# Performance work log

Hardware: AMD Instinct MI355X
Metric: run time of the kernel (lower is better)

Reference implementation:

```python
import jax, jax.numpy as jnp
import numpy as np

B, NP, FEAT, DEG, H = 16, 1024, 512, 16, 1024
E = B * NP * DEG
RATIO = 0.8


def setup_inputs() -> dict:
    key = jax.random.key(0)
    ks = jax.random.split(key, 16)
    x = jax.random.normal(ks[0], (B * NP, FEAT), jnp.float32)
    g = jnp.repeat(jnp.arange(B, dtype=jnp.int32), NP * DEG)
    src = jax.random.randint(ks[1], (E,), 0, NP, jnp.int32) + g * NP
    dst = jax.random.randint(ks[2], (E,), 0, NP, jnp.int32) + g * NP
    edge_index = jnp.stack([src, dst])
    batch = jnp.repeat(jnp.arange(B, dtype=jnp.int32), NP)
    sc = 0.02
    inp = dict(x=x, edge_index=edge_index, batch=batch)
    # SAGEConv params: out = lin_l(mean_agg) + lin_r(x); bias only on lin_l (PyG default)
    inp['W1l'] = sc * jax.random.normal(ks[3], (H, FEAT), jnp.float32)
    inp['b1'] = jnp.zeros((H,), jnp.float32)
    inp['W1r'] = sc * jax.random.normal(ks[4], (H, FEAT), jnp.float32)
    inp['p1'] = jax.random.normal(ks[5], (H,), jnp.float32)
    inp['W2l'] = sc * jax.random.normal(ks[6], (H, H), jnp.float32)
    inp['b2'] = jnp.zeros((H,), jnp.float32)
    inp['W2r'] = sc * jax.random.normal(ks[7], (H, H), jnp.float32)
    inp['p2'] = jax.random.normal(ks[8], (H,), jnp.float32)
    inp['W3l'] = sc * jax.random.normal(ks[9], (H, H), jnp.float32)
    inp['b3'] = jnp.zeros((H,), jnp.float32)
    inp['W3r'] = sc * jax.random.normal(ks[10], (H, H), jnp.float32)
    inp['p3'] = jax.random.normal(ks[11], (H,), jnp.float32)
    return inp


def _sage(x, src, dst, w, Wl, b, Wr, n_nodes):
    # mean aggregation over (masked) incoming edges, isolated nodes -> 0
    deg = jax.ops.segment_sum(w, dst, num_segments=n_nodes)
    agg = jax.ops.segment_sum(x[src] * w[:, None], dst, num_segments=n_nodes)
    mean = agg / jnp.maximum(deg, 1.0)[:, None]
    return mean @ Wl.T + b + x @ Wr.T


def _topk_pool(x, src, dst, mask, p, n_per):
    # PyG TopKPooling: score = tanh((x.w)/||w||); keep top ceil(ratio*n) per graph
    k = int(np.ceil(RATIO * n_per))
    s = jnp.tanh((x @ p) / jnp.linalg.norm(p))
    vals, idx = jax.lax.top_k(s.reshape(B, n_per), k)          # [B,k]
    old = (idx + (jnp.arange(B, dtype=idx.dtype) * n_per)[:, None]).reshape(-1)
    x_new = x[old] * vals.reshape(-1)[:, None]                  # gate kept nodes by score
    remap = jnp.full((B * n_per,), -1, jnp.int32).at[old].set(jnp.arange(B * k, dtype=jnp.int32))
    s2, d2 = remap[src], remap[dst]
    m2 = mask & (s2 >= 0) & (d2 >= 0)                           # drop edges losing an endpoint
    return x_new, jnp.where(m2, s2, 0), jnp.where(m2, d2, 0), m2, k


def _readout(x, n_per):
    xr = x.reshape(B, n_per, H)
    return jnp.concatenate([xr.max(axis=1), xr.mean(axis=1)], axis=1)  # [B, 2H]


def reference(x, edge_index, batch, W1l, b1, W1r, p1, W2l, b2, W2r, p2, W3l, b3, W3r, p3):
    src, dst = edge_index[0], edge_index[1]
    mask = jnp.ones((src.shape[0],), bool)
    n = NP
    h = jax.nn.relu(_sage(x, src, dst, mask.astype(x.dtype), W1l, b1, W1r, B * n))
    h, src, dst, mask, n = _topk_pool(h, src, dst, mask, p1, n)
    x1 = _readout(h, n)
    h = jax.nn.relu(_sage(h, src, dst, mask.astype(h.dtype), W2l, b2, W2r, B * n))
    h, src, dst, mask, n = _topk_pool(h, src, dst, mask, p2, n)
    x2 = _readout(h, n)
    h = jax.nn.relu(_sage(h, src, dst, mask.astype(h.dtype), W3l, b3, W3r, B * n))
    h, src, dst, mask, n = _topk_pool(h, src, dst, mask, p3, n)
    x3 = _readout(h, n)
    return x1 + x2 + x3
```

## Files before the change

### kernel.cpp

```cpp
#include <hip/hip_runtime.h>
#include <math.h>

#define B_    16
#define NP_   1024
#define FEAT_ 512
#define H_    1024
#define E_    262144
#define EPG_  16384
#define K1_   820
#define K2_   656
#define K3_   525
#define M1_   16384
#define M2_   13120
#define M3_   10496
#define MP1_  16384
#define MP2_  13312
#define MP3_  11264
#define SPROWS_ 16384

typedef unsigned short ushort_t;
typedef __bf16 bf16x8 __attribute__((ext_vector_type(8)));
typedef float f32x4 __attribute__((ext_vector_type(4)));

__device__ inline ushort_t f2bf(float f) {
    unsigned u = __float_as_uint(f);
    u += 0x7FFF + ((u >> 16) & 1);
    return (ushort_t)(u >> 16);
}
__device__ inline float bf2f(ushort_t h) {
    return __uint_as_float(((unsigned)h) << 16);
}
__device__ inline void split1(float v, ushort_t& hi, ushort_t& lo) {
    hi = f2bf(v);
    lo = f2bf(v - bf2f(hi));
}

__device__ inline void gll16(const void* g, void* l) {
    __builtin_amdgcn_global_load_lds((__attribute__((address_space(1))) void*)g,
                                     (__attribute__((address_space(3))) void*)l, 16, 0, 0);
}


__global__ __launch_bounds__(1024) void prep2_kernel(const int* __restrict__ ei,
                                                     int* __restrict__ counts,
                                                     int* __restrict__ offsets,
                                                     int* __restrict__ adj,
                                                     const float* __restrict__ p1,
                                                     const float* __restrict__ p2,
                                                     const float* __restrict__ p3,
                                                     float* __restrict__ pnout,
                                                     const float* __restrict__ W1l, const float* __restrict__ W1r,
                                                     const float* __restrict__ W2l, const float* __restrict__ W2r,
                                                     const float* __restrict__ W3l, const float* __restrict__ W3r,
                                                     ushort_t* __restrict__ Wb1, ushort_t* __restrict__ Wb2,
                                                     ushort_t* __restrict__ Wb3) {
    int t = threadIdx.x;
    if (blockIdx.x < 16) {
        __shared__ int cnt[1024];
        __shared__ int scanb[1024];
        int b = blockIdx.x;
        int e0 = b * EPG_;
        cnt[t] = 0;
        __syncthreads();
        for (int e = e0 + t; e < e0 + EPG_; e += 1024)
            atomicAdd(&cnt[ei[E_ + e] - b * NP_], 1);
        __syncthreads();
        int v = cnt[t];
        scanb[t] = v;
        __syncthreads();
        for (int off = 1; off < 1024; off <<= 1) {
            int tv = (t >= off) ? scanb[t - off] : 0;
            __syncthreads();
            scanb[t] += tv;
            __syncthreads();
        }
        int excl = scanb[t] - v;
        counts[b * NP_ + t] = v;
        offsets[b * NP_ + t] = e0 + excl;
        cnt[t] = excl;
        __syncthreads();
        for (int e = e0 + t; e < e0 + EPG_; e += 1024) {
            int s = ei[e];
            int dloc = ei[E_ + e] - b * NP_;
            int pos = atomicAdd(&cnt[dloc], 1);
            adj[e0 + pos] = s;
        }
        return;
    }
    if (blockIdx.x < 19) {
        const float* p = blockIdx.x == 16 ? p1 : (blockIdx.x == 17 ? p2 : p3);
        __shared__ float red[1024];
        float a = p[t];
        red[t] = a * a;
        __syncthreads();
        for (int s = 512; s > 0; s >>= 1) {
            if (t < s) red[t] += red[t + s];
            __syncthreads();
        }
        if (t == 0) pnout[blockIdx.x - 16] = sqrtf(red[0]);
        return;
    }
    int idx = (blockIdx.x - 19) * 1024 + t;
    if (idx >= 524288 + 1048576 + 1048576) return;
    const float *Wl, *Wr; ushort_t* Wbig; int K;
    if (idx < 524288) { Wl = W1l; Wr = W1r; Wbig = Wb1; K = 512; }
    else if (idx < 524288 + 1048576) { idx -= 524288; Wl = W2l; Wr = W2r; Wbig = Wb2; K = 1024; }
    else { idx -= 524288 + 1048576; Wl = W3l; Wr = W3r; Wbig = Wb3; K = 1024; }
    int n = idx / K;
    int k = idx - n * K;
    ushort_t* row = Wbig + (size_t)n * (4 * K);
    float a = Wl[idx];
    ushort_t ah = f2bf(a);
    row[k] = ah;
    row[K + k] = f2bf(a - bf2f(ah));
    float b = Wr[idx];
    ushort_t bh = f2bf(b);
    row[2 * K + k] = bh;
    row[3 * K + k] = f2bf(b - bf2f(bh));
}


__global__ __launch_bounds__(128) void agg1_k512(const float* __restrict__ x,
                                                 const int* __restrict__ adj,
                                                 const int* __restrict__ offsets,
                                                 const int* __restrict__ counts,
                                                 ushort_t* __restrict__ Abig) {
    int gid = blockIdx.x;
    int xcd = gid & 7;
    int u = gid >> 3;
    int half = u & 1;
    int pi = u >> 1;
    int gsel = (pi >= 512) ? 1 : 0;
    int g = xcd + (gsel << 3);
    int node = g * 1024 + (pi - (gsel << 9)) * 2 + (threadIdx.x >> 6);
    int c = threadIdx.x & 63;
    int col4 = half * 64 + c;
    int start = offsets[node], cnt = counts[node];
    float d = fmaxf((float)cnt, 1.0f);
    const float4* xb = (const float4*)x;
    float ax = 0.f, ay = 0.f, az = 0.f, aw = 0.f;
    int j = 0;
    for (; j + 8 <= cnt; j += 8) {
        int si[8];
#pragma unroll
        for (int q = 0; q < 8; ++q) si[q] = adj[start + j + q];
        float4 vv[8];
#pragma unroll
        for (int q = 0; q < 8; ++q) vv[q] = xb[(size_t)si[q] * 128 + col4];
#pragma unroll
        for (int q = 0; q < 8; ++q) {
            ax += vv[q].x; ay += vv[q].y; az += vv[q].z; aw += vv[q].w;
        }
    }
    for (; j + 4 <= cnt; j += 4) {
        int s0 = adj[start + j + 0], s1 = adj[start + j + 1];
        int s2 = adj[start + j + 2], s3 = adj[start + j + 3];
        float4 v0 = xb[(size_t)s0 * 128 + col4];
        float4 v1 = xb[(size_t)s1 * 128 + col4];
        float4 v2 = xb[(size_t)s2 * 128 + col4];
        float4 v3 = xb[(size_t)s3 * 128 + col4];
        ax += (v0.x + v1.x) + (v2.x + v3.x);
        ay += (v0.y + v1.y) + (v2.y + v3.y);
        az += (v0.z + v1.z) + (v2.z + v3.z);
        aw += (v0.w + v1.w) + (v2.w + v3.w);
    }
    for (; j < cnt; ++j) {
        float4 v = xb[(size_t)adj[start + j] * 128 + col4];
        ax += v.x; ay += v.y; az += v.z; aw += v.w;
    }
    float inv = 1.0f / d;
    float4 cv = xb[(size_t)node * 128 + col4];
    ushort_t* row = Abig + (size_t)node * 2048;
    int f = col4 * 4;
    ushort4 mh, ml, ch, cl;
    split1(ax * inv, mh.x, ml.x); split1(ay * inv, mh.y, ml.y);
    split1(az * inv, mh.z, ml.z); split1(aw * inv, mh.w, ml.w);
    split1(cv.x, ch.x, cl.x); split1(cv.y, ch.y, cl.y);
    split1(cv.z, ch.z, cl.z); split1(cv.w, ch.w, cl.w);
    *(ushort4*)&row[f]        = mh;
    *(ushort4*)&row[512 + f]  = ml;
    *(ushort4*)&row[1024 + f] = ch;
    *(ushort4*)&row[1536 + f] = cl;
}

template<int LAYER>
__global__ __launch_bounds__(128) void agg23_k1024(const float* __restrict__ h,
                                                   const int* __restrict__ adj,
                                                   const int* __restrict__ offsets,
                                                   const int* __restrict__ counts,
                                                   const int* __restrict__ old_idx,
                                                   const float* __restrict__ vals,
                                                   ushort_t* __restrict__ Abig,
                                                   int n_per, int M, int npad) {
    int gid = blockIdx.x;
    if (gid >= 32 * n_per) {
        int r = gid - 32 * n_per;
        if (r < npad) {
            uint4* row = (uint4*)(Abig + (size_t)(M + r) * 4096);
#pragma unroll
            for (int q = 0; q < 4; ++q) row[threadIdx.x + q * 128] = (uint4){0, 0, 0, 0};
        }
        return;
    }
    int xcd = gid & 7;
    int u = gid >> 3;
    int half = u & 1;
    int nl = u >> 1;
    int gsel = (nl >= n_per) ? 1 : 0;
    int g = xcd + (gsel << 3);
    int node = g * n_per + nl - gsel * n_per;
    int c = threadIdx.x;
    int col4 = half * 128 + c;
    int start = offsets[node], cnt = counts[node];
    float d = fmaxf((float)cnt, 1.0f);
    const float4* hb = (const float4*)h;
    float ax = 0.f, ay = 0.f, az = 0.f, aw = 0.f;
    int j = 0;
    for (; j + 8 <= cnt; j += 8) {
        int si[8];
#pragma unroll
        for (int q = 0; q < 8; ++q) si[q] = adj[start + j + q];
        int oi[8]; float wi[8];
#pragma unroll
        for (int q = 0; q < 8; ++q) { oi[q] = old_idx[si[q]]; wi[q] = vals[si[q]]; }
        float4 vv[8];
#pragma unroll
        for (int q = 0; q < 8; ++q) vv[q] = hb[(size_t)oi[q] * 256 + col4];
#pragma unroll
        for (int q = 0; q < 8; ++q) {
            ax += wi[q] * vv[q].x; ay += wi[q] * vv[q].y;
            az += wi[q] * vv[q].z; aw += wi[q] * vv[q].w;
        }
    }
    for (; j + 4 <= cnt; j += 4) {
        int s0 = adj[start + j + 0], s1 = adj[start + j + 1];
        int s2 = adj[start + j + 2], s3 = adj[start + j + 3];
        int o0 = old_idx[s0], o1 = old_idx[s1], o2 = old_idx[s2], o3 = old_idx[s3];
        float w0 = vals[s0], w1 = vals[s1], w2 = vals[s2], w3 = vals[s3];
        float4 v0 = hb[(size_t)o0 * 256 + col4];
        float4 v1 = hb[(size_t)o1 * 256 + col4];
        float4 v2 = hb[(size_t)o2 * 256 + col4];
        float4 v3 = hb[(size_t)o3 * 256 + col4];
        ax += (w0 * v0.x + w1 * v1.x) + (w2 * v2.x + w3 * v3.x);
        ay += (w0 * v0.y + w1 * v1.y) + (w2 * v2.y + w3 * v3.y);
        az += (w0 * v0.z + w1 * v1.z) + (w2 * v2.z + w3 * v3.z);
        aw += (w0 * v0.w + w1 * v1.w) + (w2 * v2.w + w3 * v3.w);
    }
    for (; j < cnt; ++j) {
        int s = adj[start + j];
        int o = old_idx[s];
        float w = vals[s];
        float4 v = hb[(size_t)o * 256 + col4];
        ax += w * v.x; ay += w * v.y; az += w * v.z; aw += w * v.w;
    }
    float inv = 1.0f / d;
    int on = old_idx[node];
    float vn = vals[node];
    float4 cv = hb[(size_t)on * 256 + col4];
    cv.x *= vn; cv.y *= vn; cv.z *= vn; cv.w *= vn;
    ushort_t* row = Abig + (size_t)node * 4096;
    int f = col4 * 4;
    ushort4 mh, ml, ch, cl;
    split1(ax * inv, mh.x, ml.x); split1(ay * inv, mh.y, ml.y);
    split1(az * inv, mh.z, ml.z); split1(aw * inv, mh.w, ml.w);
    split1(cv.x, ch.x, cl.x); split1(cv.y, ch.y, cl.y);
    split1(cv.z, ch.z, cl.z); split1(cv.w, ch.w, cl.w);
    *(ushort4*)&row[f]        = mh;
    *(ushort4*)&row[1024 + f] = ml;
    *(ushort4*)&row[2048 + f] = ch;
    *(ushort4*)&row[3072 + f] = cl;
}


#define STR_(x) #x
#define VMW2_(n) asm volatile("s_waitcnt vmcnt(" STR_(n) ")" ::: "memory")
#define VMW(n) VMW2_(n)
#define BARM() do { __builtin_amdgcn_s_barrier(); asm volatile("" ::: "memory"); } while (0)

#define STG(Lw_, pl_, src_, c_) {                                                   \
    const ushort_t* s_ = (src_) + (c_);                                             \
    gll16(s_, (Lw_) + (pl_) * 8192);                                                \
    gll16(s_ + rstep, (Lw_) + (pl_) * 8192 + 4096);                                 \
}

#define MFQ(I0, Aarr, A0, Barr)                                                     \
    _Pragma("unroll")                                                               \
    for (int ii = 0; ii < 4; ++ii) {                                                \
        _Pragma("unroll")                                                           \
        for (int jj = 0; jj < 4; ++jj)                                              \
            acc[(I0) + ii][jj] = __builtin_amdgcn_mfma_f32_16x16x32_bf16(           \
                Aarr[(A0) + ii], Barr[jj], acc[(I0) + ii][jj], 0, 0, 0);            \
    }

#define CHUNK(t_, b_, stg_) do {                                                    \
    int cs_ = ((t_) + 1 < NC2) ? ((t_) + 1) * 32 : 2 * KK + ((t_) + 1 - NC2) * 32;  \
    const ushort_t* Lr = L + (b_) * 32768;                                          \
    ushort_t* Lw = L + (1 - (b_)) * 32768 + tid * 8;                                \
    VMW(0);                                                                         \
    BARM();                                                                         \
    bf16x8 ah[8], al[8], bh[4], bl[4];                                              \
    _Pragma("unroll") for (int q = 0; q < 8; ++q)                                   \
        ah[q] = *(const bf16x8*)&Lr[aoff + q * 512];                                \
    _Pragma("unroll") for (int q = 0; q < 4; ++q)                                   \
        bh[q] = *(const bf16x8*)&Lr[16384 + boff + q * 512];                        \
    if (stg_) {                                                                     \
        STG(Lw, 0, Ag, cs_);                                                        \
        STG(Lw, 2, Bg, cs_);                                                        \
        STG(Lw, 1, Ag + KK, cs_);                                                   \
        STG(Lw, 3, Bg + KK, cs_);                                                   \
    }                                                                               \
    _Pragma("unroll") for (int q = 0; q < 8; ++q)                                   \
        al[q] = *(const bf16x8*)&Lr[8192 + aoff + q * 512];                         \
    _Pragma("unroll") for (int q = 0; q < 4; ++q)                                   \
        bl[q] = *(const bf16x8*)&Lr[24576 + boff + q * 512];                        \
    __builtin_amdgcn_s_setprio(1);                                                  \
    MFQ(0, ah, 0, bh);                                                              \
    MFQ(4, ah, 4, bh);                                                              \
    __builtin_amdgcn_s_setprio(0);                                                  \
    __builtin_amdgcn_s_setprio(1);                                                  \
    MFQ(0, al, 0, bh);                                                              \
    MFQ(4, al, 4, bh);                                                              \
    MFQ(0, ah, 0, bl);                                                              \
    MFQ(4, ah, 4, bl);                                                              \
    __builtin_amdgcn_s_setprio(0);                                                  \
} while (0)

template<int KK>
__global__ __launch_bounds__(512, 2) void gemm256(const ushort_t* __restrict__ Ab,
                                                  const ushort_t* __restrict__ Wb,
                                                  const float* __restrict__ bias,
                                                  float* __restrict__ C,
                                                  float* __restrict__ sp,
                                                  const float* __restrict__ pvec,
                                                  int npanels) {
    constexpr int LD  = 4 * KK;
    constexpr int NC  = KK / 16;
    constexpr int NC2 = KK / 32;
    __shared__ ushort_t L[65536];

    int tid = threadIdx.x;
    int lane = tid & 63;
    int w = tid >> 6;
    int wm = w >> 2, wn = w & 3;

    int nb = npanels * 4;
    int per = nb >> 3;
    int bp = (blockIdx.x & 7) * per + (blockIdx.x >> 3);
    int panel = bp >> 2, cb = bp & 3;
    int m0 = panel * 256, n0 = cb * 256;

    int srow = tid >> 2;
    int gq = (tid & 3) ^ (srow & 3) ^ ((srow >> 2) & 3);
    const ushort_t* Ag = Ab + (size_t)(m0 + srow) * LD + gq * 8;
    const ushort_t* Bg = Wb + (size_t)(n0 + srow) * LD + gq * 8;
    const size_t rstep = (size_t)128 * LD;

    int qsw = (lane >> 4) ^ (lane & 3) ^ ((lane >> 2) & 3);
    int aoff = (wm * 128 + (lane & 15)) * 32 + qsw * 8;
    int boff = (wn * 64 + (lane & 15)) * 32 + qsw * 8;

    f32x4 acc[8][4];
#pragma unroll
    for (int i = 0; i < 8; ++i)
#pragma unroll
        for (int j = 0; j < 4; ++j) acc[i][j] = (f32x4){0.f, 0.f, 0.f, 0.f};

    {
        ushort_t* Lw0 = L + tid * 8;
        STG(Lw0, 0, Ag, 0);
        STG(Lw0, 2, Bg, 0);
        STG(Lw0, 1, Ag + KK, 0);
        STG(Lw0, 3, Bg + KK, 0);
    }

#pragma unroll 1
    for (int t = 0; t < NC - 2; t += 2) {
        CHUNK(t,     0, 1);
        CHUNK(t + 1, 1, 1);
    }
    CHUNK(NC - 2, 0, 1);
    CHUNK(NC - 1, 1, 0);

    float bj[4], pj[4];
#pragma unroll
    for (int j = 0; j < 4; ++j) {
        int col = n0 + wn * 64 + j * 16 + (lane & 15);
        bj[j] = bias[col];
        pj[j] = pvec[col];
    }
    int slot = cb * 4 + wn;
#pragma unroll
    for (int i = 0; i < 8; ++i) {
        int row0 = m0 + wm * 128 + i * 16 + (lane >> 4) * 4;
        float sacc[4] = {0.f, 0.f, 0.f, 0.f};
#pragma unroll
        for (int j = 0; j < 4; ++j) {
            int col = n0 + wn * 64 + j * 16 + (lane & 15);
#pragma unroll
            for (int r = 0; r < 4; ++r) {
                float v = acc[i][j][r] + bj[j];
                v = v > 0.f ? v : 0.f;
                C[(size_t)(row0 + r) * 1024 + col] = v;
                sacc[r] += v * pj[j];
            }
        }
#pragma unroll
        for (int r = 0; r < 4; ++r) {
            float sv_ = sacc[r];
            sv_ += __shfl_xor(sv_, 1);
            sv_ += __shfl_xor(sv_, 2);
            sv_ += __shfl_xor(sv_, 4);
            sv_ += __shfl_xor(sv_, 8);
            if ((lane & 15) == 0) sp[slot * SPROWS_ + row0 + r] = sv_;
        }
    }
}


template<int FIRST>
__global__ __launch_bounds__(1024) void tail_kernel(const float* __restrict__ sp,
                                                    const float* __restrict__ pn,
                                                    const float* __restrict__ h,
                                                    float* __restrict__ out,
                                                    int n, int k,
                                                    int* __restrict__ old_idx, float* __restrict__ vals,
                                                    const int* __restrict__ ei,
                                                    int* __restrict__ esrc, int* __restrict__ edst,
                                                    int* __restrict__ emask,
                                                    int* __restrict__ counts, int* __restrict__ offsets,
                                                    int* __restrict__ adj, int do_edges) {
    __shared__ float sv[1024];
    __shared__ int   rmap[1024];
    __shared__ int   oi_s[1024];
    __shared__ float vv_s[1024];
    __shared__ float4 rmx[32][32];
    __shared__ float4 rsm[32][32];
    int b = blockIdx.x / 9, role = blockIdx.x % 9;
    int t = threadIdx.x;
    if (role == 8 && !do_edges) return;

    float mine = -INFINITY;
    if (t < n) {
        int base = b * n + t;
        float s0 = 0.f;
#pragma unroll
        for (int c = 0; c < 16; ++c) s0 += sp[c * SPROWS_ + base];
        mine = s0;
    }
    sv[t] = mine;
    __syncthreads();
    int rank = 0;
#pragma unroll 4
    for (int j = 0; j < 1024; ++j) {
        float o = sv[j];
        rank += (o > mine) || (o == mine && j < t);
    }
    bool kept = (t < n) && (rank < k);
    rmap[t] = kept ? rank : -1;
    if (kept) {
        float tv = tanhf(mine / pn[0]);
        oi_s[rank] = b * n + t;
        vv_s[rank] = tv;
        if (role == 8) {
            old_idx[b * k + rank] = b * n + t;
            vals[b * k + rank] = tv;
        }
    }
    __syncthreads();

    if (role < 8) {
        int c32 = t & 31, g = t >> 5;
        int col4 = role * 32 + c32;
        const float4* hb = (const float4*)h;
        float4 mx = {-INFINITY, -INFINITY, -INFINITY, -INFINITY};
        float4 sm = {0.f, 0.f, 0.f, 0.f};
        for (int i = g; i < k; i += 32) {
            int o = oi_s[i];
            float wgt = vv_s[i];
            float4 v = hb[(size_t)o * 256 + col4];
            v.x *= wgt; v.y *= wgt; v.z *= wgt; v.w *= wgt;
            mx.x = fmaxf(mx.x, v.x); mx.y = fmaxf(mx.y, v.y);
            mx.z = fmaxf(mx.z, v.z); mx.w = fmaxf(mx.w, v.w);
            sm.x += v.x; sm.y += v.y; sm.z += v.z; sm.w += v.w;
        }
        rmx[g][c32] = mx; rsm[g][c32] = sm;
        __syncthreads();
        for (int s = 16; s > 0; s >>= 1) {
            if (g < s) {
                float4 om = rmx[g + s][c32], os = rsm[g + s][c32];
                float4 m = rmx[g][c32], ss2 = rsm[g][c32];
                m.x = fmaxf(m.x, om.x); m.y = fmaxf(m.y, om.y);
                m.z = fmaxf(m.z, om.z); m.w = fmaxf(m.w, om.w);
                ss2.x += os.x; ss2.y += os.y; ss2.z += os.z; ss2.w += os.w;
                rmx[g][c32] = m; rsm[g][c32] = ss2;
            }
            __syncthreads();
        }
        if (g == 0) {
            float4 m = rmx[0][c32], ss2 = rsm[0][c32];
            float invk = 1.0f / (float)k;
            float* o0 = out + (size_t)b * 2048 + col4 * 4;
            float* o1 = o0 + 1024;
            if (FIRST) {
                o0[0] = m.x; o0[1] = m.y; o0[2] = m.z; o0[3] = m.w;
                o1[0] = ss2.x * invk; o1[1] = ss2.y * invk;
                o1[2] = ss2.z * invk; o1[3] = ss2.w * invk;
            } else {
                o0[0] += m.x; o0[1] += m.y; o0[2] += m.z; o0[3] += m.w;
                o1[0] += ss2.x * invk; o1[1] += ss2.y * invk;
                o1[2] += ss2.z * invk; o1[3] += ss2.w * invk;
            }
        }
        return;
    }

    __shared__ int cnt_s[1024];
    cnt_s[t] = 0;
    __syncthreads();
    int e0 = b * EPG_;
    for (int e = e0 + t; e < e0 + EPG_; e += 1024) {
        int ms = FIRST ? 1 : emask[e];
        if (ms) {
            int s = FIRST ? ei[e] : esrc[e];
            int dd = FIRST ? ei[E_ + e] : edst[e];
            int ns = rmap[s - b * n];
            int nd = rmap[dd - b * n];
            if (ns >= 0 && nd >= 0) atomicAdd(&cnt_s[nd], 1);
        }
    }
    __syncthreads();
    int v = (t < k) ? cnt_s[t] : 0;
    oi_s[t] = v;
    __syncthreads();
    for (int off = 1; off < 1024; off <<= 1) {
        int tv = (t >= off) ? oi_s[t - off] : 0;
        __syncthreads();
        oi_s[t] += tv;
        __syncthreads();
    }
    int excl = oi_s[t] - v;
    if (t < k) {
        counts[b * k + t] = v;
        offsets[b * k + t] = e0 + excl;
        cnt_s[t] = excl;
    }
    __syncthreads();
    for (int e = e0 + t; e < e0 + EPG_; e += 1024) {
        int ms = FIRST ? 1 : emask[e];
        if (ms) {
            int s = FIRST ? ei[e] : esrc[e];
            int dd = FIRST ? ei[E_ + e] : edst[e];
            int ns = rmap[s - b * n];
            int nd = rmap[dd - b * n];
            if (ns >= 0 && nd >= 0) {
                int gs = b * k + ns;
                esrc[e] = gs;
                edst[e] = b * k + nd;
                if (FIRST) emask[e] = 1;
                int pos = atomicAdd(&cnt_s[nd], 1);
                adj[e0 + pos] = gs;
            } else {
                emask[e] = 0;
            }
        } else if (FIRST) {
            emask[e] = 0;
        }
    }
}


extern "C" void kernel_launch(void* const* d_in, const int* in_sizes, int n_in,
                              void* d_out, int out_size, void* d_ws, size_t ws_size,
                              hipStream_t stream) {
    const float* x   = (const float*)d_in[0];
    const int*   ei  = (const int*)d_in[1];
    const float* W1l = (const float*)d_in[3];
    const float* b1  = (const float*)d_in[4];
    const float* W1r = (const float*)d_in[5];
    const float* p1  = (const float*)d_in[6];
    const float* W2l = (const float*)d_in[7];
    const float* b2  = (const float*)d_in[8];
    const float* W2r = (const float*)d_in[9];
    const float* p2  = (const float*)d_in[10];
    const float* W3l = (const float*)d_in[11];
    const float* b3  = (const float*)d_in[12];
    const float* W3r = (const float*)d_in[13];
    const float* p3  = (const float*)d_in[14];
    float* out = (float*)d_out;

    char* ws = (char*)d_ws;
    size_t off = 0;
    float* bufOut = (float*)(ws + off); off += (size_t)MP1_ * 1024 * 4;
    ushort_t* Abig = (ushort_t*)(ws + off); off += (size_t)MP2_ * 4096 * 2;
    ushort_t* Wb1 = (ushort_t*)(ws + off); off += (size_t)1024 * 2048 * 2;
    ushort_t* Wb2 = (ushort_t*)(ws + off); off += (size_t)1024 * 4096 * 2;
    ushort_t* Wb3 = (ushort_t*)(ws + off); off += (size_t)1024 * 4096 * 2;
    float* sp = (float*)(ws + off); off += (size_t)16 * SPROWS_ * 4;
    char* misc = ws + off;
    int*   counts = (int*)(misc + 0 * 65536);
    int*   offsets= (int*)(misc + 1 * 65536);
    int*   old_idx= (int*)(misc + 2 * 65536);
    float* vals   = (float*)(misc + 3 * 65536);
    float* pnormv = (float*)(misc + 4 * 65536);
    int*   adj    = (int*)(misc + 5 * 65536);
    int*   esrc   = (int*)(misc + 5 * 65536 + 1 * 1048576);
    int*   edst   = (int*)(misc + 5 * 65536 + 2 * 1048576);
    int*   emask  = (int*)(misc + 5 * 65536 + 3 * 1048576);

    prep2_kernel<<<19 + (524288 + 2 * 1048576) / 1024, 1024, 0, stream>>>(
        ei, counts, offsets, adj, p1, p2, p3, pnormv,
        W1l, W1r, W2l, W2r, W3l, W3r, Wb1, Wb2, Wb3);

    agg1_k512<<<16384, 128, 0, stream>>>(x, adj, offsets, counts, Abig);
    gemm256<512><<<(MP1_ / 256) * 4, 512, 0, stream>>>(Abig, Wb1, b1, bufOut, sp, p1, MP1_ / 256);
    tail_kernel<1><<<B_ * 9, 1024, 0, stream>>>(sp, pnormv + 0, bufOut, out, NP_, K1_,
                                                old_idx, vals, ei, esrc, edst, emask,
                                                counts, offsets, adj, 1);

    agg23_k1024<2><<<32 * K1_ + (MP2_ - M2_), 128, 0, stream>>>(
        bufOut, adj, offsets, counts, old_idx, vals, Abig, K1_, M2_, MP2_ - M2_);
    gemm256<1024><<<(MP2_ / 256) * 4, 512, 0, stream>>>(Abig, Wb2, b2, bufOut, sp, p2, MP2_ / 256);
    tail_kernel<0><<<B_ * 9, 1024, 0, stream>>>(sp, pnormv + 1, bufOut, out, K1_, K2_,
                                                old_idx, vals, ei, esrc, edst, emask,
                                                counts, offsets, adj, 1);

    agg23_k1024<3><<<32 * K2_ + (MP3_ - M3_), 128, 0, stream>>>(
        bufOut, adj, offsets, counts, old_idx, vals, Abig, K2_, M3_, MP3_ - M3_);
    gemm256<1024><<<(MP3_ / 256) * 4, 512, 0, stream>>>(Abig, Wb3, b3, bufOut, sp, p3, MP3_ / 256);
    tail_kernel<0><<<B_ * 9, 1024, 0, stream>>>(sp, pnormv + 2, bufOut, out, K2_, K3_,
                                                old_idx, vals, ei, esrc, edst, emask,
                                                counts, offsets, adj, 0);
}
```

Baseline: 752.3 us.

## Prefetch next chunk's LDS fragments across barrier in GEMM main loop

Restructures the double-buffered GEMM chunk so the wait-for-global-loads and barrier move mid-chunk, after the first MFMA batch. The first half-fragments (ah/bh) for the next chunk are read from the other LDS buffer right after the barrier and held in ping-pong register arrays. This aims to hide LDS read latency and barrier stalls behind MFMA work. It costs extra VGPRs for the second fragment set, which at 512 threads and 2 blocks per CU could cause spills or lower occupancy.

```diff
diff --git a/kernel.cpp b/kernel.cpp
--- a/kernel.cpp
+++ b/kernel.cpp
@@ -292,36 +292,39 @@
                 Aarr[(A0) + ii], Barr[jj], acc[(I0) + ii][jj], 0, 0, 0);            \
     }
 
-#define CHUNK(t_, b_, stg_) do {                                                    \
+#define CHUNK(t_, b_, stg_, pre_, XA, XB, YA, YB) do {                              \
     int cs_ = ((t_) + 1 < NC2) ? ((t_) + 1) * 32 : 2 * KK + ((t_) + 1 - NC2) * 32;  \
     const ushort_t* Lr = L + (b_) * 32768;                                          \
+    const ushort_t* Lq = L + (1 - (b_)) * 32768;                                    \
     ushort_t* Lw = L + (1 - (b_)) * 32768 + tid * 8;                                \
-    VMW(0);                                                                         \
-    BARM();                                                                         \
-    bf16x8 ah[8], al[8], bh[4], bl[4];                                              \
+    bf16x8 al[8], bl[4];                                                            \
     _Pragma("unroll") for (int q = 0; q < 8; ++q)                                   \
-        ah[q] = *(const bf16x8*)&Lr[aoff + q * 512];                                \
+        al[q] = *(const bf16x8*)&Lr[8192 + aoff + q * 512];                         \
     _Pragma("unroll") for (int q = 0; q < 4; ++q)                                   \
-        bh[q] = *(const bf16x8*)&Lr[16384 + boff + q * 512];                        \
+        bl[q] = *(const bf16x8*)&Lr[24576 + boff + q * 512];                        \
     if (stg_) {                                                                     \
         STG(Lw, 0, Ag, cs_);                                                        \
         STG(Lw, 2, Bg, cs_);                                                        \
         STG(Lw, 1, Ag + KK, cs_);                                                   \
         STG(Lw, 3, Bg + KK, cs_);                                                   \
     }                                                                               \
-    _Pragma("unroll") for (int q = 0; q < 8; ++q)                                   \
-        al[q] = *(const bf16x8*)&Lr[8192 + aoff + q * 512];                         \
-    _Pragma("unroll") for (int q = 0; q < 4; ++q)                                   \
-        bl[q] = *(const bf16x8*)&Lr[24576 + boff + q * 512];                        \
     __builtin_amdgcn_s_setprio(1);                                                  \
-    MFQ(0, ah, 0, bh);                                                              \
-    MFQ(4, ah, 4, bh);                                                              \
+    MFQ(0, XA, 0, XB);                                                              \
+    MFQ(4, XA, 4, XB);                                                              \
+    MFQ(0, al, 0, XB);                                                              \
+    MFQ(4, al, 4, XB);                                                              \
     __builtin_amdgcn_s_setprio(0);                                                  \
+    VMW(0);                                                                         \
+    BARM();                                                                         \
+    if (pre_) {                                                                     \
+        _Pragma("unroll") for (int q = 0; q < 8; ++q)                               \
+            YA[q] = *(const bf16x8*)&Lq[aoff + q * 512];                            \
+        _Pragma("unroll") for (int q = 0; q < 4; ++q)                               \
+            YB[q] = *(const bf16x8*)&Lq[16384 + boff + q * 512];                    \
+    }                                                                               \
     __builtin_amdgcn_s_setprio(1);                                                  \
-    MFQ(0, al, 0, bh);                                                              \
-    MFQ(4, al, 4, bh);                                                              \
-    MFQ(0, ah, 0, bl);                                                              \
-    MFQ(4, ah, 4, bl);                                                              \
+    MFQ(0, XA, 0, bl);                                                              \
+    MFQ(4, XA, 4, bl);                                                              \
     __builtin_amdgcn_s_setprio(0);                                                  \
 } while (0)
 
@@ -365,21 +368,29 @@
 #pragma unroll
         for (int j = 0; j < 4; ++j) acc[i][j] = (f32x4){0.f, 0.f, 0.f, 0.f};
 
+    bf16x8 ahA[8], bhA[4], ahB[8], bhB[4];
+
     {
         ushort_t* Lw0 = L + tid * 8;
         STG(Lw0, 0, Ag, 0);
         STG(Lw0, 2, Bg, 0);
         STG(Lw0, 1, Ag + KK, 0);
         STG(Lw0, 3, Bg + KK, 0);
+        VMW(0);
+        BARM();
+#pragma unroll
+        for (int q = 0; q < 8; ++q) ahA[q] = *(const bf16x8*)&L[aoff + q * 512];
+#pragma unroll
+        for (int q = 0; q < 4; ++q) bhA[q] = *(const bf16x8*)&L[16384 + boff + q * 512];
     }
 
 #pragma unroll 1
     for (int t = 0; t < NC - 2; t += 2) {
-        CHUNK(t,     0, 1);
-        CHUNK(t + 1, 1, 1);
-    }
-    CHUNK(NC - 2, 0, 1);
-    CHUNK(NC - 1, 1, 0);
+        CHUNK(t,     0, 1, 1, ahA, bhA, ahB, bhB);
+        CHUNK(t + 1, 1, 1, 1, ahB, bhB, ahA, bhA);
+    }
+    CHUNK(NC - 2, 0, 1, 1, ahA, bhA, ahB, bhB);
+    CHUNK(NC - 1, 1, 0, 0, ahB, bhB, ahA, bhA);
 
     float bj[4], pj[4];
 #pragma unroll
```

Result: no change. 747.9 us, median of 3 (-0.6%).
